# Kernel optimization log

Measured on AMD Instinct MI355X. Metric: run time of the kernel, lower is better.

Reference implementation:

```python
import jax, jax.numpy as jnp
import numpy as np

B, I, H, AH, AI = 4096, 1024, 1024, 128, 16
EPS = 1e-5  # nn.LayerNorm default


def _ln(x, w, b):
    mu = jnp.mean(x, -1, keepdims=True)
    var = jnp.mean((x - mu) ** 2, -1, keepdims=True)
    return (x - mu) * jax.lax.rsqrt(var + EPS) * w + b


def setup_inputs() -> dict:
    key = jax.random.key(0)
    ks = jax.random.split(key, 12)
    d = {}
    d['x'] = jax.random.normal(ks[0], (B, I), jnp.float32)
    d['total_h'] = jax.random.normal(ks[1], (B, H + AH), jnp.float32)
    d['total_c'] = jax.random.normal(ks[2], (B, H + AH), jnp.float32)
    # main cell params
    d['w_ih'] = jax.random.normal(ks[3], (4 * H, I), jnp.float32) * 0.02
    d['w_hh'] = jax.random.normal(ks[4], (4 * H, H), jnp.float32) * 0.02
    d['b_ih'] = jnp.zeros((4 * H,), jnp.float32)
    d['b_hh'] = jnp.zeros((4 * H,), jnp.float32)
    d['ln_i_w'] = jnp.ones((4 * H,), jnp.float32); d['ln_i_b'] = jnp.zeros((4 * H,), jnp.float32)
    d['ln_h_w'] = jnp.ones((4 * H,), jnp.float32); d['ln_h_b'] = jnp.zeros((4 * H,), jnp.float32)
    d['ln_c_w'] = jnp.ones((H,), jnp.float32); d['ln_c_b'] = jnp.zeros((H,), jnp.float32)
    # 8 AdaptiveNorm modules, stacked on leading axis (order ix,jx,fx,ox,ih,jh,fh,oh)
    d['norm_zw_w'] = jax.random.normal(ks[5], (8, AI, AH), jnp.float32) * 0.05
    d['norm_zw_b'] = jnp.ones((8, AI), jnp.float32)
    d['norm_alpha_w'] = jax.random.normal(ks[6], (8, H, AI), jnp.float32) * (0.1 / AI)
    # 8 AdaptiveBias modules, stacked (order ixb,jxb,fxb,oxb,ihb,jhb,fhb,ohb)
    d['bias_zb_w'] = jax.random.normal(ks[7], (8, AI, AH), jnp.float32) * 0.01
    d['bias_beta_w'] = jax.random.normal(ks[8], (8, H, AI), jnp.float32) * 0.01
    # adaptive LayerNormLSTMCell (input = I+H, hidden = AH)
    d['a_w_ih'] = jax.random.normal(ks[9], (4 * AH, I + H), jnp.float32) * 0.02
    d['a_w_hh'] = jax.random.normal(ks[10], (4 * AH, AH), jnp.float32) * 0.02
    d['a_ln_i_w'] = jnp.ones((4 * AH,), jnp.float32); d['a_ln_i_b'] = jnp.zeros((4 * AH,), jnp.float32)
    d['a_ln_h_w'] = jnp.ones((4 * AH,), jnp.float32); d['a_ln_h_b'] = jnp.zeros((4 * AH,), jnp.float32)
    d['a_ln_c_w'] = jnp.ones((AH,), jnp.float32); d['a_ln_c_b'] = jnp.zeros((AH,), jnp.float32)
    return d


def _forward(x, total_h, total_c, w_ih, w_hh, b_ih, b_hh, ln_i_w, ln_i_b,
             ln_h_w, ln_h_b, ln_c_w, ln_c_b, norm_zw_w, norm_zw_b,
             norm_alpha_w, bias_zb_w, bias_beta_w, a_w_ih, a_w_hh,
             a_ln_i_w, a_ln_i_b, a_ln_h_w, a_ln_h_b, a_ln_c_w, a_ln_c_b):
    hx, ah = total_h[:, :H], total_h[:, H:]
    cx, ac = total_c[:, :H], total_c[:, H:]
    # ---- adaptive LayerNormLSTMCell (hypernetwork) ----
    ai = jnp.concatenate([x, hx], axis=1)                     # [B, I+H]
    ig = _ln(ai @ a_w_ih.T, a_ln_i_w, a_ln_i_b)               # [B, 4*AH]
    hg = _ln(ah @ a_w_hh.T, a_ln_h_w, a_ln_h_b)
    g = ig + hg
    gi, gf, gj, go = jnp.split(g, 4, axis=1)                  # ingate, forget, cell, out
    acy = _ln(jax.nn.sigmoid(gf) * ac + jax.nn.sigmoid(gi) * jnp.tanh(gj), a_ln_c_w, a_ln_c_b)
    ada = jax.nn.sigmoid(go) * jnp.tanh(acy)                  # adaptive_output [B, AH]
    # ---- 8 AdaptiveNorm scales + 8 AdaptiveBias offsets, batched ----
    zw = jnp.einsum('ba,sia->bsi', ada, norm_zw_w) + norm_zw_b  # [B,8,AI]
    alpha = jnp.einsum('bsi,shi->bsh', zw, norm_alpha_w)        # [B,8,H]
    zb = jnp.einsum('ba,sia->bsi', ada, bias_zb_w)              # [B,8,AI]
    beta = jnp.einsum('bsi,shi->bsh', zb, bias_beta_w)          # [B,8,H]
    xh = (x @ w_ih.T).reshape(-1, 4, H)                         # chunks ix,jx,fx,ox
    hh = (hx @ w_hh.T).reshape(-1, 4, H)                        # chunks ih,jh,fh,oh
    in_g = (xh * alpha[:, :4] + b_ih.reshape(4, H) + beta[:, :4]).reshape(-1, 4 * H)
    hid_g = (hh * alpha[:, 4:] + b_hh.reshape(4, H) + beta[:, 4:]).reshape(-1, 4 * H)
    # ---- cell_operate ----
    gates = _ln(in_g, ln_i_w, ln_i_b) + _ln(hid_g, ln_h_w, ln_h_b)
    i, j, f, o = jnp.split(gates, 4, axis=1)                  # in, cell, forget, out
    cy = _ln(jax.nn.sigmoid(f) * cx + jax.nn.sigmoid(i) * jnp.tanh(j), ln_c_w, ln_c_b)
    hy = jax.nn.sigmoid(o) * jnp.tanh(cy)
    new_total_h = jnp.concatenate([hy, ada], axis=1)
    new_total_c = jnp.concatenate([cy, acy], axis=1)
    return hy, new_total_h, new_total_c


def reference(x, total_h, total_c, w_ih, w_hh, b_ih, b_hh, ln_i_w, ln_i_b,
              ln_h_w, ln_h_b, ln_c_w, ln_c_b, norm_zw_w, norm_zw_b,
              norm_alpha_w, bias_zb_w, bias_beta_w, a_w_ih, a_w_hh,
              a_ln_i_w, a_ln_i_b, a_ln_h_w, a_ln_h_b, a_ln_c_w, a_ln_c_b):
    return _forward(x, total_h, total_c, w_ih, w_hh, b_ih, b_hh, ln_i_w, ln_i_b,
                    ln_h_w, ln_h_b, ln_c_w, ln_c_b, norm_zw_w, norm_zw_b,
                    norm_alpha_w, bias_zb_w, bias_beta_w, a_w_ih, a_w_hh,
                    a_ln_i_w, a_ln_i_b, a_ln_h_w, a_ln_h_b, a_ln_c_w, a_ln_c_b)
```

## Files before the change

### kernel.cpp

```cpp
#include <hip/hip_runtime.h>
#include <cstdint>
#include <cstddef>


#define B_   4096
#define I_   1024
#define H_   1024
#define AH_  128
#define G4_  4096
#define EPS_ 1e-5f

#define OUT_TH ((size_t)B_ * H_)
#define OUT_TC (OUT_TH + (size_t)B_ * (H_ + AH_))

typedef short s16x8 __attribute__((ext_vector_type(8)));
typedef float f32x4 __attribute__((ext_vector_type(4)));

__device__ __forceinline__ unsigned short f2bf_rn(float f) {
    unsigned int u = __builtin_bit_cast(unsigned int, f);
    unsigned int r = u + 0x7FFFu + ((u >> 16) & 1u);
    return (unsigned short)(r >> 16);
}
__device__ __forceinline__ float bf2f(unsigned short h) {
    unsigned int u = ((unsigned int)h) << 16;
    return __builtin_bit_cast(float, u);
}
__device__ __forceinline__ float sigf(float x) { return 1.0f / (1.0f + expf(-x)); }

__device__ __forceinline__ void gld16(const void* g, void* l) {
    __builtin_amdgcn_global_load_lds(
        (const __attribute__((address_space(1))) unsigned int*)g,
        (__attribute__((address_space(3))) unsigned int*)l,
        16, 0, 0);
}

__global__ void split8_kernel(const float* __restrict__ src, int srcStride, int srcOff,
                              long nThreads, int kshift,
                              unsigned short* __restrict__ dst, int dstStride,
                              int offHi, int offLo) {
    long t = (long)blockIdx.x * blockDim.x + threadIdx.x;
    if (t >= nThreads) return;
    int r  = (int)(t >> kshift);
    int kk = ((int)t & ((1 << kshift) - 1)) * 8;
    const float* sp = src + (size_t)r * srcStride + srcOff + kk;
    f32x4 v0 = *(const f32x4*)sp;
    f32x4 v1 = *(const f32x4*)(sp + 4);
    float v[8] = {v0[0], v0[1], v0[2], v0[3], v1[0], v1[1], v1[2], v1[3]};
    s16x8 hi, lo;
#pragma unroll
    for (int j = 0; j < 8; ++j) {
        unsigned short hu = f2bf_rn(v[j]);
        unsigned short lu = f2bf_rn(v[j] - bf2f(hu));
        hi[j] = (short)hu; lo[j] = (short)lu;
    }
    size_t base = (size_t)r * dstStride + kk;
    *(s16x8*)(dst + base + offHi) = hi;
    *(s16x8*)(dst + base + offLo) = lo;
}

__global__ void transpose128_kernel(const float* __restrict__ zw_w, const float* __restrict__ zb_w,
                                    float* __restrict__ ZWT, float* __restrict__ ZBT) {
    int t = blockIdx.x * 256 + threadIdx.x;
    int idx = t >> 7, a = t & 127;
    ZWT[a * 128 + idx] = zw_w[idx * 128 + a];
    ZBT[a * 128 + idx] = zb_w[idx * 128 + a];
}

__launch_bounds__(256, 2)
__global__ void gemm_bt_bf16(const unsigned short* __restrict__ A0,
                             const unsigned short* __restrict__ A1,
                             int lda,
                             const unsigned short* __restrict__ W, int ldw, int wzOff,
                             float* __restrict__ C, int ldc, long czOff,
                             int K, int kA1, int kW1) {
    __shared__ __align__(16) unsigned short As[128 * 32];
    __shared__ __align__(16) unsigned short Bs[128 * 32];
    const unsigned short* A  = blockIdx.z ? A1 : A0;
    const unsigned short* Wp = W + (size_t)blockIdx.z * wzOff;
    float* Cp = C + (size_t)blockIdx.z * czOff;

    const int gx = gridDim.x;
    int lin = blockIdx.y * gx + blockIdx.x;
    const int cpx = (gx * gridDim.y) >> 3;
    lin = (lin & 7) * cpx + (lin >> 3);
    const int bx = lin % gx, by = lin / gx;

    const int tid  = threadIdx.x;
    const int lane = tid & 63;
    const int w    = tid >> 6;
    const int wr   = w >> 1, wc = w & 1;
    const int l15  = lane & 15;
    const int lk   = (lane >> 4) * 8;

    f32x4 acc[4][4] = {};

    for (int kt = 0; kt < K; kt += 32) {
        const unsigned short* Ab = A  + (kt < kA1 ? kt : kt - kA1);
        const unsigned short* Wb = Wp + (kt < kW1 ? kt : kt - kW1);
#pragma unroll
        for (int it = 0; it < 2; ++it) {
            int q = it * 256 + tid;
            int row = q >> 2, c8 = (q & 3) * 8;
            gld16(Ab + (size_t)(by * 128 + row) * lda + c8,
                  (char*)As + (size_t)(it * 256 + w * 64) * 16);
        }
#pragma unroll
        for (int it = 0; it < 2; ++it) {
            int q = it * 256 + tid;
            int row = q >> 2, c8 = (q & 3) * 8;
            gld16(Wb + (size_t)(bx * 128 + row) * ldw + c8,
                  (char*)Bs + (size_t)(it * 256 + w * 64) * 16);
        }
        __syncthreads();

        s16x8 afr[4], bfr[4];
#pragma unroll
        for (int m = 0; m < 4; ++m)
            afr[m] = *(const s16x8*)&As[(wr * 64 + m * 16 + l15) * 32 + lk];
#pragma unroll
        for (int n = 0; n < 4; ++n)
            bfr[n] = *(const s16x8*)&Bs[(wc * 64 + n * 16 + l15) * 32 + lk];
#pragma unroll
        for (int m = 0; m < 4; ++m)
#pragma unroll
            for (int n = 0; n < 4; ++n)
                acc[m][n] = __builtin_amdgcn_mfma_f32_16x16x32_bf16(
                    afr[m], bfr[n], acc[m][n], 0, 0, 0);
        __syncthreads();
    }

    const int r0 = by * 128 + wr * 64;
    const int c0 = bx * 128 + wc * 64;
    const int rl = (lane >> 4) * 4;
#pragma unroll
    for (int m = 0; m < 4; ++m)
#pragma unroll
        for (int n = 0; n < 4; ++n)
#pragma unroll
            for (int j = 0; j < 4; ++j)
                Cp[(size_t)(r0 + m * 16 + rl + j) * ldc + c0 + n * 16 + l15] = acc[m][n][j];
}

__launch_bounds__(64)
__global__ void adaptive_gates_kernel(const float* __restrict__ IGa, const float* __restrict__ IGb,
                                      const float* __restrict__ HG,
                                      const float* __restrict__ total_c,
                                      const float* __restrict__ alniw, const float* __restrict__ alnib,
                                      const float* __restrict__ alnhw, const float* __restrict__ alnhb,
                                      const float* __restrict__ alncw, const float* __restrict__ alncb,
                                      const float* __restrict__ ZWT, const float* __restrict__ zw_b,
                                      const float* __restrict__ ZBT,
                                      float* __restrict__ ZW, float* __restrict__ ZB,
                                      float* __restrict__ out) {
    const int b    = blockIdx.x;
    const int lane = threadIdx.x;
    __shared__ float ada_lds[AH_];

    float ig[8], hg[8];
    const float* ipa = IGa + (size_t)b * 512 + lane * 8;
    const float* ipb = IGb + (size_t)b * 512 + lane * 8;
    const float* hgp = HG  + (size_t)b * 512 + lane * 8;
    float sI = 0, qI = 0, sH = 0, qH = 0;
#pragma unroll
    for (int j = 0; j < 8; ++j) {
        ig[j] = ipa[j] + ipb[j]; sI += ig[j]; qI += ig[j] * ig[j];
        hg[j] = hgp[j];          sH += hg[j]; qH += hg[j] * hg[j];
    }
#pragma unroll
    for (int m = 1; m < 64; m <<= 1) {
        sI += __shfl_xor(sI, m); qI += __shfl_xor(qI, m);
        sH += __shfl_xor(sH, m); qH += __shfl_xor(qH, m);
    }
    const float muI = sI * (1.0f / 512.0f);
    const float rI  = rsqrtf(qI * (1.0f / 512.0f) - muI * muI + EPS_);
    const float muH = sH * (1.0f / 512.0f);
    const float rH  = rsqrtf(qH * (1.0f / 512.0f) - muH * muH + EPS_);

    float g[8];
#pragma unroll
    for (int j = 0; j < 8; ++j) {
        int c = lane * 8 + j;
        g[j] = (ig[j] - muI) * rI * alniw[c] + alnib[c]
             + (hg[j] - muH) * rH * alnhw[c] + alnhb[c];
    }

    const int l15 = lane & 15;
    float cp[8], gov[8];
    float s = 0, q = 0;
#pragma unroll
    for (int j = 0; j < 8; ++j) {
        float giv = __shfl(g[j], l15);
        float gfv = __shfl(g[j], 16 + l15);
        float gjv = __shfl(g[j], 32 + l15);
        gov[j]    = __shfl(g[j], 48 + l15);
        int a = l15 * 8 + j;
        float ac = total_c[(size_t)b * (H_ + AH_) + H_ + a];
        cp[j] = sigf(gfv) * ac + sigf(giv) * tanhf(gjv);
        s += cp[j]; q += cp[j] * cp[j];
    }
#pragma unroll
    for (int m = 1; m < 16; m <<= 1) { s += __shfl_xor(s, m); q += __shfl_xor(q, m); }
    const float mu = s * (1.0f / 128.0f);
    const float rs = rsqrtf(q * (1.0f / 128.0f) - mu * mu + EPS_);

    float adav[8], acyv[8];
#pragma unroll
    for (int j = 0; j < 8; ++j) {
        int a = l15 * 8 + j;
        acyv[j] = (cp[j] - mu) * rs * alncw[a] + alncb[a];
        adav[j] = sigf(gov[j]) * tanhf(acyv[j]);
    }
    if (lane < 16) {
#pragma unroll
        for (int j = 0; j < 8; ++j) {
            int a = lane * 8 + j;
            ada_lds[a] = adav[j];
            out[OUT_TH + (size_t)b * (H_ + AH_) + H_ + a] = adav[j];
            out[OUT_TC + (size_t)b * (H_ + AH_) + H_ + a] = acyv[j];
        }
    }
    __syncthreads();

    float az0 = 0, az1 = 0, ab0 = 0, ab1 = 0;
#pragma unroll 4
    for (int a = 0; a < 128; ++a) {
        float ad = ada_lds[a];
        float2 wz = *(const float2*)&ZWT[a * 128 + lane * 2];
        float2 wb = *(const float2*)&ZBT[a * 128 + lane * 2];
        az0 += ad * wz.x; az1 += ad * wz.y;
        ab0 += ad * wb.x; ab1 += ad * wb.y;
    }
    const int i0 = lane * 2, i1 = lane * 2 + 1;
    ZW[(size_t)b * 128 + i0] = az0 + zw_b[i0];
    ZW[(size_t)b * 128 + i1] = az1 + zw_b[i1];
    ZB[(size_t)b * 128 + i0] = ab0;
    ZB[(size_t)b * 128 + i1] = ab1;
}

__launch_bounds__(512)
__global__ void scale_stats_kernel(float* __restrict__ XH, float* __restrict__ HH,
                                   const float* __restrict__ ZW, const float* __restrict__ ZB,
                                   const float* __restrict__ aw, const float* __restrict__ bw,
                                   const float* __restrict__ b_ih, const float* __restrict__ b_hh,
                                   float* __restrict__ STATS) {
    const int tid  = threadIdx.x;
    const int lane = tid & 63;
    const int w    = tid >> 6;
    const int b0   = blockIdx.x * 8;

    __shared__ __align__(16) float zwl[8 * 128], zbl[8 * 128];
    __shared__ float part[8][8][4];
    __shared__ float tot[8][4];

    for (int t = tid; t < 1024; t += 512) {
        int r = t >> 7, si = t & 127;
        zwl[t] = ZW[(size_t)(b0 + r) * 128 + si];
        zbl[t] = ZB[(size_t)(b0 + r) * 128 + si];
    }
    __syncthreads();

    float sI[8] = {}, qI[8] = {}, sH[8] = {}, qH[8] = {};

    for (int strip = w; strip < 128; strip += 8) {
        const bool isIn = strip < 64;
        const int  c    = (isIn ? strip : strip - 64) * 64 + lane;
        const int  se   = (c >> 10) + (isIn ? 0 : 4);
        float*       X    = isIn ? XH : HH;
        const float* bias = isIn ? b_ih : b_hh;
        const int    h    = c & 1023;

        const f32x4* awp = (const f32x4*)(aw + ((size_t)se * 1024 + h) * 16);
        const f32x4* bwp = (const f32x4*)(bw + ((size_t)se * 1024 + h) * 16);
        f32x4 a0 = awp[0], a1 = awp[1], a2 = awp[2], a3 = awp[3];
        f32x4 w0 = bwp[0], w1 = bwp[1], w2 = bwp[2], w3 = bwp[3];
        const float bc = bias[c];

#pragma unroll
        for (int r = 0; r < 8; ++r) {
            const f32x4* zp = (const f32x4*)&zwl[r * 128 + se * 16];
            const f32x4* yp = (const f32x4*)&zbl[r * 128 + se * 16];
            f32x4 z0 = zp[0], z1 = zp[1], z2 = zp[2], z3 = zp[3];
            f32x4 y0 = yp[0], y1 = yp[1], y2 = yp[2], y3 = yp[3];
            float alpha = a0[0]*z0[0] + a0[1]*z0[1] + a0[2]*z0[2] + a0[3]*z0[3]
                        + a1[0]*z1[0] + a1[1]*z1[1] + a1[2]*z1[2] + a1[3]*z1[3]
                        + a2[0]*z2[0] + a2[1]*z2[1] + a2[2]*z2[2] + a2[3]*z2[3]
                        + a3[0]*z3[0] + a3[1]*z3[1] + a3[2]*z3[2] + a3[3]*z3[3];
            float beta  = w0[0]*y0[0] + w0[1]*y0[1] + w0[2]*y0[2] + w0[3]*y0[3]
                        + w1[0]*y1[0] + w1[1]*y1[1] + w1[2]*y1[2] + w1[3]*y1[3]
                        + w2[0]*y2[0] + w2[1]*y2[1] + w2[2]*y2[2] + w2[3]*y2[3]
                        + w3[0]*y3[0] + w3[1]*y3[1] + w3[2]*y3[2] + w3[3]*y3[3];
            size_t off = (size_t)(b0 + r) * G4_ + c;
            float v = X[off] * alpha + bc + beta;
            X[off] = v;
            if (isIn) { sI[r] += v; qI[r] += v * v; }
            else      { sH[r] += v; qH[r] += v * v; }
        }
    }

#pragma unroll
    for (int r = 0; r < 8; ++r) {
#pragma unroll
        for (int m = 1; m < 64; m <<= 1) {
            sI[r] += __shfl_xor(sI[r], m); qI[r] += __shfl_xor(qI[r], m);
            sH[r] += __shfl_xor(sH[r], m); qH[r] += __shfl_xor(qH[r], m);
        }
        if (lane == 0) {
            part[w][r][0] = sI[r]; part[w][r][1] = qI[r];
            part[w][r][2] = sH[r]; part[w][r][3] = qH[r];
        }
    }
    __syncthreads();
    if (tid < 32) {
        int r = tid >> 2, cmp = tid & 3;
        float t = 0;
        for (int ww = 0; ww < 8; ++ww) t += part[ww][r][cmp];
        tot[r][cmp] = t;
    }
    __syncthreads();
    if (tid < 8) {
        int r = tid;
        float muI = tot[r][0] * (1.0f / 4096.0f);
        float vI  = tot[r][1] * (1.0f / 4096.0f) - muI * muI;
        float muH = tot[r][2] * (1.0f / 4096.0f);
        float vH  = tot[r][3] * (1.0f / 4096.0f) - muH * muH;
        f32x4 st = { muI, rsqrtf(vI + EPS_), muH, rsqrtf(vH + EPS_) };
        *(f32x4*)(STATS + (size_t)(b0 + r) * 4) = st;
    }
}

__launch_bounds__(256)
__global__ void final_gates_kernel(const float* __restrict__ XH, const float* __restrict__ HH,
                                   const float* __restrict__ STATS,
                                   const float* __restrict__ lniw, const float* __restrict__ lnib,
                                   const float* __restrict__ lnhw, const float* __restrict__ lnhb,
                                   const float* __restrict__ lncw, const float* __restrict__ lncb,
                                   const float* __restrict__ total_c,
                                   float* __restrict__ out) {
    const int b = blockIdx.x, tid = threadIdx.x;
    const int lane = tid & 63, w = tid >> 6;
    __shared__ float red[4][2];

    const f32x4 st = *(const f32x4*)(STATS + (size_t)b * 4);
    const int h0 = tid * 4;

    float gg[4][4];
#pragma unroll
    for (int s = 0; s < 4; ++s) {
        int c = s * 1024 + h0;
        f32x4 xi = *(const f32x4*)(XH + (size_t)b * G4_ + c);
        f32x4 hi = *(const f32x4*)(HH + (size_t)b * G4_ + c);
        f32x4 wi = *(const f32x4*)(lniw + c);
        f32x4 bi = *(const f32x4*)(lnib + c);
        f32x4 wh = *(const f32x4*)(lnhw + c);
        f32x4 bh = *(const f32x4*)(lnhb + c);
#pragma unroll
        for (int e = 0; e < 4; ++e)
            gg[s][e] = (xi[e] - st[0]) * st[1] * wi[e] + bi[e]
                     + (hi[e] - st[2]) * st[3] * wh[e] + bh[e];
    }

    float cp[4], ov[4];
    float s_ = 0, q_ = 0;
#pragma unroll
    for (int e = 0; e < 4; ++e) {
        float iv = gg[0][e], jv = gg[1][e], fv = gg[2][e];
        ov[e] = gg[3][e];
        float cx = total_c[(size_t)b * (H_ + AH_) + h0 + e];
        cp[e] = sigf(fv) * cx + sigf(iv) * tanhf(jv);
        s_ += cp[e]; q_ += cp[e] * cp[e];
    }
#pragma unroll
    for (int m = 1; m < 64; m <<= 1) { s_ += __shfl_xor(s_, m); q_ += __shfl_xor(q_, m); }
    if (lane == 0) { red[w][0] = s_; red[w][1] = q_; }
    __syncthreads();
    float S = red[0][0] + red[1][0] + red[2][0] + red[3][0];
    float Q = red[0][1] + red[1][1] + red[2][1] + red[3][1];
    float mu = S * (1.0f / 1024.0f);
    float rs = rsqrtf(Q * (1.0f / 1024.0f) - mu * mu + EPS_);

    f32x4 hyv, cyv;
#pragma unroll
    for (int e = 0; e < 4; ++e) {
        int h = h0 + e;
        float cy = (cp[e] - mu) * rs * lncw[h] + lncb[h];
        float hy = sigf(ov[e]) * tanhf(cy);
        cyv[e] = cy; hyv[e] = hy;
    }
    *(f32x4*)(out + (size_t)b * H_ + h0)                  = hyv;
    *(f32x4*)(out + OUT_TH + (size_t)b * (H_ + AH_) + h0) = hyv;
    *(f32x4*)(out + OUT_TC + (size_t)b * (H_ + AH_) + h0) = cyv;
}

extern "C" void kernel_launch(void* const* d_in, const int* in_sizes, int n_in,
                              void* d_out, int out_size, void* d_ws, size_t ws_size,
                              hipStream_t stream) {
    const float* x          = (const float*)d_in[0];
    const float* total_h    = (const float*)d_in[1];
    const float* total_c    = (const float*)d_in[2];
    const float* w_ih       = (const float*)d_in[3];
    const float* w_hh       = (const float*)d_in[4];
    const float* b_ih       = (const float*)d_in[5];
    const float* b_hh       = (const float*)d_in[6];
    const float* ln_i_w     = (const float*)d_in[7];
    const float* ln_i_b     = (const float*)d_in[8];
    const float* ln_h_w     = (const float*)d_in[9];
    const float* ln_h_b     = (const float*)d_in[10];
    const float* ln_c_w     = (const float*)d_in[11];
    const float* ln_c_b     = (const float*)d_in[12];
    const float* norm_zw_w  = (const float*)d_in[13];
    const float* norm_zw_b  = (const float*)d_in[14];
    const float* norm_alpha_w = (const float*)d_in[15];
    const float* bias_zb_w  = (const float*)d_in[16];
    const float* bias_beta_w = (const float*)d_in[17];
    const float* a_w_ih     = (const float*)d_in[18];
    const float* a_w_hh     = (const float*)d_in[19];
    const float* a_ln_i_w   = (const float*)d_in[20];
    const float* a_ln_i_b   = (const float*)d_in[21];
    const float* a_ln_h_w   = (const float*)d_in[22];
    const float* a_ln_h_b   = (const float*)d_in[23];
    const float* a_ln_c_w   = (const float*)d_in[24];
    const float* a_ln_c_b   = (const float*)d_in[25];
    float* out = (float*)d_out;

    char* ws = (char*)d_ws;
    unsigned short* XA  = (unsigned short*)(ws + 0);
    unsigned short* HXA = (unsigned short*)(ws + 16777216);
    unsigned short* WIH = (unsigned short*)(ws + 33554432);
    unsigned short* WHH = (unsigned short*)(ws + 50331648);
    unsigned short* WAI = (unsigned short*)(ws + 67108864);
    unsigned short* AHS = (unsigned short*)(ws + 71303168);
    unsigned short* WAH = (unsigned short*)(ws + 73400320);
    float* IG    = (float*)(ws + 73662464);
    float* HG    = (float*)(ws + 90439680);
    float* XHp   = (float*)(ws + 98828288);
    float* HHp   = (float*)(ws + 165937152);
    float* ZW    = (float*)(ws + 233046016);
    float* ZB    = (float*)(ws + 235143168);
    float* STATS = (float*)(ws + 237240320);
    float* ZWT   = (float*)(ws + 237305856);
    float* ZBT   = (float*)(ws + 237371392);

    auto grid8 = [](long n) { return dim3((unsigned)((n / 8 + 255) / 256)); };

    split8_kernel<<<grid8(4096L*1024), 256, 0, stream>>>(x,       1024, 0,    4096L*128, 7, XA,  2048, 0, 1024);
    split8_kernel<<<grid8(4096L*1024), 256, 0, stream>>>(total_h, 1152, 0,    4096L*128, 7, HXA, 2048, 0, 1024);
    split8_kernel<<<grid8(4096L*128),  256, 0, stream>>>(total_h, 1152, 1024, 4096L*16,  4, AHS, 256,  0, 128);
    split8_kernel<<<grid8(4096L*1024), 256, 0, stream>>>(w_ih,    1024, 0,    4096L*128, 7, WIH, 2048, 0, 1024);
    split8_kernel<<<grid8(4096L*1024), 256, 0, stream>>>(w_hh,    1024, 0,    4096L*128, 7, WHH, 2048, 0, 1024);
    split8_kernel<<<grid8(512L*1024),  256, 0, stream>>>(a_w_ih,  2048, 0,    512L*128,  7, WAI, 4096, 0,    1024);
    split8_kernel<<<grid8(512L*1024),  256, 0, stream>>>(a_w_ih,  2048, 1024, 512L*128,  7, WAI, 4096, 2048, 3072);
    split8_kernel<<<grid8(512L*128),   256, 0, stream>>>(a_w_hh,  128,  0,    512L*16,   4, WAH, 256,  0, 128);
    transpose128_kernel<<<64, 256, 0, stream>>>(norm_zw_w, bias_zb_w, ZWT, ZBT);

    gemm_bt_bf16<<<dim3(4, 32, 2), 256, 0, stream>>>(XA, HXA, 2048, WAI, 4096, 2048, IG, 512, 4096L*512, 3072, 1024, 2048);
    gemm_bt_bf16<<<dim3(4, 32, 1), 256, 0, stream>>>(AHS, AHS, 256, WAH, 256, 0, HG, 512, 0, 384, 128, 256);
    gemm_bt_bf16<<<dim3(32, 32, 1), 256, 0, stream>>>(XA,  XA,  2048, WIH, 2048, 0, XHp, 4096, 0, 3072, 1024, 2048);
    gemm_bt_bf16<<<dim3(32, 32, 1), 256, 0, stream>>>(HXA, HXA, 2048, WHH, 2048, 0, HHp, 4096, 0, 3072, 1024, 2048);

    adaptive_gates_kernel<<<4096, 64, 0, stream>>>(IG, IG + 4096L*512, HG, total_c,
        a_ln_i_w, a_ln_i_b, a_ln_h_w, a_ln_h_b, a_ln_c_w, a_ln_c_b,
        ZWT, norm_zw_b, ZBT, ZW, ZB, out);

    scale_stats_kernel<<<512, 512, 0, stream>>>(XHp, HHp, ZW, ZB,
        norm_alpha_w, bias_beta_w, b_ih, b_hh, STATS);

    final_gates_kernel<<<4096, 256, 0, stream>>>(XHp, HHp, STATS,
        ln_i_w, ln_i_b, ln_h_w, ln_h_b, ln_c_w, ln_c_b, total_c, out);
}
```

Measured before the change: 668.6 us.

## Fuse adaptive scale/bias and LayerNorm partial stats into main GEMM epilogue

The scale_stats kernel is removed. Its per-column alpha/beta scaling, bias add and row sum/sumsq partials move into the epilogue of the two large GEMMs, which are now merged into one z=2 launch that runs after the adaptive gates kernel. This saves a full read-modify-write pass over the two 64MB gate buffers and one launch. The final kernel reduces 128 partial pairs per row to get mean and rstd. The cost is a heavier epilogue with extra global loads of alpha/beta weights, and the big GEMMs can no longer overlap with the adaptive path.

```diff
diff --git a/kernel.cpp b/kernel.cpp
--- a/kernel.cpp
+++ b/kernel.cpp
@@ -26,6 +26,9 @@
     return __builtin_bit_cast(float, u);
 }
 __device__ __forceinline__ float sigf(float x) { return 1.0f / (1.0f + expf(-x)); }
+__device__ __forceinline__ float dot4(f32x4 a, f32x4 b) {
+    return a[0]*b[0] + a[1]*b[1] + a[2]*b[2] + a[3]*b[3];
+}
 
 __device__ __forceinline__ void gld16(const void* g, void* l) {
     __builtin_amdgcn_global_load_lds(
@@ -72,12 +75,17 @@
                              int lda,
                              const unsigned short* __restrict__ W, int ldw, int wzOff,
                              float* __restrict__ C, int ldc, long czOff,
-                             int K, int kA1, int kW1) {
+                             int K, int kA1, int kW1,
+                             const float* __restrict__ ZW, const float* __restrict__ ZB,
+                             const float* __restrict__ aw, const float* __restrict__ bw,
+                             const float* __restrict__ biasX, const float* __restrict__ biasH,
+                             float* __restrict__ PART) {
     __shared__ __align__(16) unsigned short As[128 * 32];
     __shared__ __align__(16) unsigned short Bs[128 * 32];
-    const unsigned short* A  = blockIdx.z ? A1 : A0;
-    const unsigned short* Wp = W + (size_t)blockIdx.z * wzOff;
-    float* Cp = C + (size_t)blockIdx.z * czOff;
+    const int z = blockIdx.z;
+    const unsigned short* A  = z ? A1 : A0;
+    const unsigned short* Wp = W + (size_t)z * wzOff;
+    float* Cp = C + (size_t)z * czOff;
 
     const int gx = gridDim.x;
     int lin = blockIdx.y * gx + blockIdx.x;
@@ -91,6 +99,7 @@
     const int wr   = w >> 1, wc = w & 1;
     const int l15  = lane & 15;
     const int lk   = (lane >> 4) * 8;
+    const int rl   = (lane >> 4) * 4;
 
     f32x4 acc[4][4] = {};
 
@@ -129,16 +138,83 @@
         __syncthreads();
     }
 
-    const int r0 = by * 128 + wr * 64;
-    const int c0 = bx * 128 + wc * 64;
-    const int rl = (lane >> 4) * 4;
-#pragma unroll
-    for (int m = 0; m < 4; ++m)
-#pragma unroll
-        for (int n = 0; n < 4; ++n)
-#pragma unroll
-            for (int j = 0; j < 4; ++j)
-                Cp[(size_t)(r0 + m * 16 + rl + j) * ldc + c0 + n * 16 + l15] = acc[m][n][j];
+    if (PART == nullptr) {
+        const int r0 = by * 128 + wr * 64;
+        const int c0 = bx * 128 + wc * 64;
+#pragma unroll
+        for (int m = 0; m < 4; ++m)
+#pragma unroll
+            for (int n = 0; n < 4; ++n)
+#pragma unroll
+                for (int j = 0; j < 4; ++j)
+                    Cp[(size_t)(r0 + m * 16 + rl + j) * ldc + c0 + n * 16 + l15] = acc[m][n][j];
+        return;
+    }
+
+    const int se = (z ? 4 : 0) + (bx >> 3);
+    float* zwl = (float*)As;
+    float* zbl = (float*)Bs;
+    {
+        int rr = tid >> 1, ii = (tid & 1) * 8;
+        const float* zp = ZW + (size_t)(by * 128 + rr) * 128 + se * 16 + ii;
+        const float* yp = ZB + (size_t)(by * 128 + rr) * 128 + se * 16 + ii;
+        f32x4 za = *(const f32x4*)zp, zc = *(const f32x4*)(zp + 4);
+        f32x4 ya = *(const f32x4*)yp, yc = *(const f32x4*)(yp + 4);
+        *(f32x4*)&zwl[rr * 16 + ii]     = za;
+        *(f32x4*)&zwl[rr * 16 + ii + 4] = zc;
+        *(f32x4*)&zbl[rr * 16 + ii]     = ya;
+        *(f32x4*)&zbl[rr * 16 + ii + 4] = yc;
+    }
+    __syncthreads();
+
+    const float* bias = z ? biasH : biasX;
+#pragma unroll
+    for (int half = 0; half < 2; ++half) {
+        f32x4 awv[2][4], bwv[2][4];
+        float bcv[2];
+        int   ccol[2];
+#pragma unroll
+        for (int t = 0; t < 2; ++t) {
+            int cc = bx * 128 + wc * 64 + (half * 2 + t) * 16 + l15;
+            ccol[t] = cc;
+            int h = cc & 1023;
+            const f32x4* ap = (const f32x4*)(aw + ((size_t)se * 1024 + h) * 16);
+            const f32x4* bp = (const f32x4*)(bw + ((size_t)se * 1024 + h) * 16);
+            awv[t][0] = ap[0]; awv[t][1] = ap[1]; awv[t][2] = ap[2]; awv[t][3] = ap[3];
+            bwv[t][0] = bp[0]; bwv[t][1] = bp[1]; bwv[t][2] = bp[2]; bwv[t][3] = bp[3];
+            bcv[t] = bias[cc];
+        }
+#pragma unroll
+        for (int m = 0; m < 4; ++m)
+#pragma unroll
+        for (int j = 0; j < 4; ++j) {
+            const int rloc = wr * 64 + m * 16 + rl + j;
+            const f32x4* zp = (const f32x4*)&zwl[rloc * 16];
+            const f32x4* yp = (const f32x4*)&zbl[rloc * 16];
+            f32x4 z0 = zp[0], z1 = zp[1], z2 = zp[2], z3 = zp[3];
+            f32x4 y0 = yp[0], y1 = yp[1], y2 = yp[2], y3 = yp[3];
+            float s = 0, q = 0;
+#pragma unroll
+            for (int t = 0; t < 2; ++t) {
+                float alpha = dot4(z0, awv[t][0]) + dot4(z1, awv[t][1])
+                            + dot4(z2, awv[t][2]) + dot4(z3, awv[t][3]);
+                float beta  = dot4(y0, bwv[t][0]) + dot4(y1, bwv[t][1])
+                            + dot4(y2, bwv[t][2]) + dot4(y3, bwv[t][3]);
+                float v = acc[m][half * 2 + t][j] * alpha + bcv[t] + beta;
+                Cp[(size_t)(by * 128 + rloc) * ldc + ccol[t]] = v;
+                s += v; q += v * v;
+            }
+#pragma unroll
+            for (int msk = 1; msk < 16; msk <<= 1) {
+                s += __shfl_xor(s, msk); q += __shfl_xor(q, msk);
+            }
+            if (l15 == 0) {
+                int cb = bx * 4 + wc * 2 + half;
+                float2 pr = { s, q };
+                *(float2*)&PART[(((size_t)z * 4096 + by * 128 + rloc) * 128 + cb) * 2] = pr;
+            }
+        }
+    }
 }
 
 __launch_bounds__(64)
@@ -237,100 +313,9 @@
     ZB[(size_t)b * 128 + i1] = ab1;
 }
 
-__launch_bounds__(512)
-__global__ void scale_stats_kernel(float* __restrict__ XH, float* __restrict__ HH,
-                                   const float* __restrict__ ZW, const float* __restrict__ ZB,
-                                   const float* __restrict__ aw, const float* __restrict__ bw,
-                                   const float* __restrict__ b_ih, const float* __restrict__ b_hh,
-                                   float* __restrict__ STATS) {
-    const int tid  = threadIdx.x;
-    const int lane = tid & 63;
-    const int w    = tid >> 6;
-    const int b0   = blockIdx.x * 8;
-
-    __shared__ __align__(16) float zwl[8 * 128], zbl[8 * 128];
-    __shared__ float part[8][8][4];
-    __shared__ float tot[8][4];
-
-    for (int t = tid; t < 1024; t += 512) {
-        int r = t >> 7, si = t & 127;
-        zwl[t] = ZW[(size_t)(b0 + r) * 128 + si];
-        zbl[t] = ZB[(size_t)(b0 + r) * 128 + si];
-    }
-    __syncthreads();
-
-    float sI[8] = {}, qI[8] = {}, sH[8] = {}, qH[8] = {};
-
-    for (int strip = w; strip < 128; strip += 8) {
-        const bool isIn = strip < 64;
-        const int  c    = (isIn ? strip : strip - 64) * 64 + lane;
-        const int  se   = (c >> 10) + (isIn ? 0 : 4);
-        float*       X    = isIn ? XH : HH;
-        const float* bias = isIn ? b_ih : b_hh;
-        const int    h    = c & 1023;
-
-        const f32x4* awp = (const f32x4*)(aw + ((size_t)se * 1024 + h) * 16);
-        const f32x4* bwp = (const f32x4*)(bw + ((size_t)se * 1024 + h) * 16);
-        f32x4 a0 = awp[0], a1 = awp[1], a2 = awp[2], a3 = awp[3];
-        f32x4 w0 = bwp[0], w1 = bwp[1], w2 = bwp[2], w3 = bwp[3];
-        const float bc = bias[c];
-
-#pragma unroll
-        for (int r = 0; r < 8; ++r) {
-            const f32x4* zp = (const f32x4*)&zwl[r * 128 + se * 16];
-            const f32x4* yp = (const f32x4*)&zbl[r * 128 + se * 16];
-            f32x4 z0 = zp[0], z1 = zp[1], z2 = zp[2], z3 = zp[3];
-            f32x4 y0 = yp[0], y1 = yp[1], y2 = yp[2], y3 = yp[3];
-            float alpha = a0[0]*z0[0] + a0[1]*z0[1] + a0[2]*z0[2] + a0[3]*z0[3]
-                        + a1[0]*z1[0] + a1[1]*z1[1] + a1[2]*z1[2] + a1[3]*z1[3]
-                        + a2[0]*z2[0] + a2[1]*z2[1] + a2[2]*z2[2] + a2[3]*z2[3]
-                        + a3[0]*z3[0] + a3[1]*z3[1] + a3[2]*z3[2] + a3[3]*z3[3];
-            float beta  = w0[0]*y0[0] + w0[1]*y0[1] + w0[2]*y0[2] + w0[3]*y0[3]
-                        + w1[0]*y1[0] + w1[1]*y1[1] + w1[2]*y1[2] + w1[3]*y1[3]
-                        + w2[0]*y2[0] + w2[1]*y2[1] + w2[2]*y2[2] + w2[3]*y2[3]
-                        + w3[0]*y3[0] + w3[1]*y3[1] + w3[2]*y3[2] + w3[3]*y3[3];
-            size_t off = (size_t)(b0 + r) * G4_ + c;
-            float v = X[off] * alpha + bc + beta;
-            X[off] = v;
-            if (isIn) { sI[r] += v; qI[r] += v * v; }
-            else      { sH[r] += v; qH[r] += v * v; }
-        }
-    }
-
-#pragma unroll
-    for (int r = 0; r < 8; ++r) {
-#pragma unroll
-        for (int m = 1; m < 64; m <<= 1) {
-            sI[r] += __shfl_xor(sI[r], m); qI[r] += __shfl_xor(qI[r], m);
-            sH[r] += __shfl_xor(sH[r], m); qH[r] += __shfl_xor(qH[r], m);
-        }
-        if (lane == 0) {
-            part[w][r][0] = sI[r]; part[w][r][1] = qI[r];
-            part[w][r][2] = sH[r]; part[w][r][3] = qH[r];
-        }
-    }
-    __syncthreads();
-    if (tid < 32) {
-        int r = tid >> 2, cmp = tid & 3;
-        float t = 0;
-        for (int ww = 0; ww < 8; ++ww) t += part[ww][r][cmp];
-        tot[r][cmp] = t;
-    }
-    __syncthreads();
-    if (tid < 8) {
-        int r = tid;
-        float muI = tot[r][0] * (1.0f / 4096.0f);
-        float vI  = tot[r][1] * (1.0f / 4096.0f) - muI * muI;
-        float muH = tot[r][2] * (1.0f / 4096.0f);
-        float vH  = tot[r][3] * (1.0f / 4096.0f) - muH * muH;
-        f32x4 st = { muI, rsqrtf(vI + EPS_), muH, rsqrtf(vH + EPS_) };
-        *(f32x4*)(STATS + (size_t)(b0 + r) * 4) = st;
-    }
-}
-
 __launch_bounds__(256)
 __global__ void final_gates_kernel(const float* __restrict__ XH, const float* __restrict__ HH,
-                                   const float* __restrict__ STATS,
+                                   const float* __restrict__ PART,
                                    const float* __restrict__ lniw, const float* __restrict__ lnib,
                                    const float* __restrict__ lnhw, const float* __restrict__ lnhb,
                                    const float* __restrict__ lncw, const float* __restrict__ lncb,
@@ -339,10 +324,23 @@
     const int b = blockIdx.x, tid = threadIdx.x;
     const int lane = tid & 63, w = tid >> 6;
     __shared__ float red[4][2];
-
-    const f32x4 st = *(const f32x4*)(STATS + (size_t)b * 4);
+    __shared__ float red2[2][2];
+
+    if (w < 2) {
+        const float* pz = PART + ((size_t)w * 4096 + b) * 256;
+        f32x4 v = *(const f32x4*)(pz + lane * 4);
+        float s = v[0] + v[2], q = v[1] + v[3];
+#pragma unroll
+        for (int m = 1; m < 64; m <<= 1) { s += __shfl_xor(s, m); q += __shfl_xor(q, m); }
+        if (lane == 0) { red2[w][0] = s; red2[w][1] = q; }
+    }
+    __syncthreads();
+    const float muI = red2[0][0] * (1.0f / 4096.0f);
+    const float rI  = rsqrtf(red2[0][1] * (1.0f / 4096.0f) - muI * muI + EPS_);
+    const float muH = red2[1][0] * (1.0f / 4096.0f);
+    const float rH  = rsqrtf(red2[1][1] * (1.0f / 4096.0f) - muH * muH + EPS_);
+
     const int h0 = tid * 4;
-
     float gg[4][4];
 #pragma unroll
     for (int s = 0; s < 4; ++s) {
@@ -355,8 +353,8 @@
         f32x4 bh = *(const f32x4*)(lnhb + c);
 #pragma unroll
         for (int e = 0; e < 4; ++e)
-            gg[s][e] = (xi[e] - st[0]) * st[1] * wi[e] + bi[e]
-                     + (hi[e] - st[2]) * st[3] * wh[e] + bh[e];
+            gg[s][e] = (xi[e] - muI) * rI * wi[e] + bi[e]
+                     + (hi[e] - muH) * rH * wh[e] + bh[e];
     }
 
     float cp[4], ov[4];
@@ -436,9 +434,9 @@
     float* HHp   = (float*)(ws + 165937152);
     float* ZW    = (float*)(ws + 233046016);
     float* ZB    = (float*)(ws + 235143168);
-    float* STATS = (float*)(ws + 237240320);
-    float* ZWT   = (float*)(ws + 237305856);
-    float* ZBT   = (float*)(ws + 237371392);
+    float* ZWT   = (float*)(ws + 237240320);
+    float* ZBT   = (float*)(ws + 237305856);
+    float* PART  = (float*)(ws + 237371392);
 
     auto grid8 = [](long n) { return dim3((unsigned)((n / 8 + 255) / 256)); };
 
@@ -452,18 +450,21 @@
     split8_kernel<<<grid8(512L*128),   256, 0, stream>>>(a_w_hh,  128,  0,    512L*16,   4, WAH, 256,  0, 128);
     transpose128_kernel<<<64, 256, 0, stream>>>(norm_zw_w, bias_zb_w, ZWT, ZBT);
 
-    gemm_bt_bf16<<<dim3(4, 32, 2), 256, 0, stream>>>(XA, HXA, 2048, WAI, 4096, 2048, IG, 512, 4096L*512, 3072, 1024, 2048);
-    gemm_bt_bf16<<<dim3(4, 32, 1), 256, 0, stream>>>(AHS, AHS, 256, WAH, 256, 0, HG, 512, 0, 384, 128, 256);
-    gemm_bt_bf16<<<dim3(32, 32, 1), 256, 0, stream>>>(XA,  XA,  2048, WIH, 2048, 0, XHp, 4096, 0, 3072, 1024, 2048);
-    gemm_bt_bf16<<<dim3(32, 32, 1), 256, 0, stream>>>(HXA, HXA, 2048, WHH, 2048, 0, HHp, 4096, 0, 3072, 1024, 2048);
+    gemm_bt_bf16<<<dim3(4, 32, 2), 256, 0, stream>>>(XA, HXA, 2048, WAI, 4096, 2048,
+        IG, 512, 4096L*512, 3072, 1024, 2048,
+        nullptr, nullptr, nullptr, nullptr, nullptr, nullptr, nullptr);
+    gemm_bt_bf16<<<dim3(4, 32, 1), 256, 0, stream>>>(AHS, AHS, 256, WAH, 256, 0,
+        HG, 512, 0, 384, 128, 256,
+        nullptr, nullptr, nullptr, nullptr, nullptr, nullptr, nullptr);
 
     adaptive_gates_kernel<<<4096, 64, 0, stream>>>(IG, IG + 4096L*512, HG, total_c,
         a_ln_i_w, a_ln_i_b, a_ln_h_w, a_ln_h_b, a_ln_c_w, a_ln_c_b,
         ZWT, norm_zw_b, ZBT, ZW, ZB, out);
 
-    scale_stats_kernel<<<512, 512, 0, stream>>>(XHp, HHp, ZW, ZB,
-        norm_alpha_w, bias_beta_w, b_ih, b_hh, STATS);
-
-    final_gates_kernel<<<4096, 256, 0, stream>>>(XHp, HHp, STATS,
+    gemm_bt_bf16<<<dim3(32, 32, 2), 256, 0, stream>>>(XA, HXA, 2048, WIH, 2048, 8388608,
+        XHp, 4096, 16777216, 3072, 1024, 2048,
+        ZW, ZB, norm_alpha_w, bias_beta_w, b_ih, b_hh, PART);
+
+    final_gates_kernel<<<4096, 256, 0, stream>>>(XHp, HHp, PART,
         ln_i_w, ln_i_b, ln_h_w, ln_h_b, ln_c_w, ln_c_b, total_c, out);
 }
```

Measured after the change: 723.1 us. +8.1%, slower.

## Fuse split/transpose prep into one kernel and widen scale_stats to two columns per lane

Applied to the files above, without the earlier changes.

Merges the eight bf16 hi/lo split launches and the transpose launch into a single prep kernel that dispatches on block index, removing per-launch overhead and tail gaps. The scale_stats kernel now has each lane handle two adjacent columns with float2 loads and stores, reusing the shared-memory z vectors across both columns and halving the strip loop count. The big GEMMs are also reordered to run after the adaptive-gates kernel. The costs are more registers per thread in scale_stats and a larger branchy prep grid.

```diff
diff --git a/kernel.cpp b/kernel.cpp
--- a/kernel.cpp
+++ b/kernel.cpp
@@ -26,6 +26,9 @@
     return __builtin_bit_cast(float, u);
 }
 __device__ __forceinline__ float sigf(float x) { return 1.0f / (1.0f + expf(-x)); }
+__device__ __forceinline__ float dot4(f32x4 a, f32x4 b) {
+    return a[0]*b[0] + a[1]*b[1] + a[2]*b[2] + a[3]*b[3];
+}
 
 __device__ __forceinline__ void gld16(const void* g, void* l) {
     __builtin_amdgcn_global_load_lds(
@@ -34,14 +37,12 @@
         16, 0, 0);
 }
 
-__global__ void split8_kernel(const float* __restrict__ src, int srcStride, int srcOff,
-                              long nThreads, int kshift,
-                              unsigned short* __restrict__ dst, int dstStride,
-                              int offHi, int offLo) {
-    long t = (long)blockIdx.x * blockDim.x + threadIdx.x;
-    if (t >= nThreads) return;
-    int r  = (int)(t >> kshift);
-    int kk = ((int)t & ((1 << kshift) - 1)) * 8;
+__device__ __forceinline__ void split_body(const float* __restrict__ src, int srcStride,
+                                           int srcOff, int kshift,
+                                           unsigned short* __restrict__ dst, int dstStride,
+                                           int offHi, int offLo, int t) {
+    int r  = t >> kshift;
+    int kk = (t & ((1 << kshift) - 1)) * 8;
     const float* sp = src + (size_t)r * srcStride + srcOff + kk;
     f32x4 v0 = *(const f32x4*)sp;
     f32x4 v1 = *(const f32x4*)(sp + 4);
@@ -58,12 +59,38 @@
     *(s16x8*)(dst + base + offLo) = lo;
 }
 
-__global__ void transpose128_kernel(const float* __restrict__ zw_w, const float* __restrict__ zb_w,
-                                    float* __restrict__ ZWT, float* __restrict__ ZBT) {
-    int t = blockIdx.x * 256 + threadIdx.x;
-    int idx = t >> 7, a = t & 127;
-    ZWT[a * 128 + idx] = zw_w[idx * 128 + a];
-    ZBT[a * 128 + idx] = zb_w[idx * 128 + a];
+__global__ void prep_kernel(const float* __restrict__ x, const float* __restrict__ total_h,
+                            const float* __restrict__ w_ih, const float* __restrict__ w_hh,
+                            const float* __restrict__ a_w_ih, const float* __restrict__ a_w_hh,
+                            const float* __restrict__ zw_w, const float* __restrict__ zb_w,
+                            unsigned short* __restrict__ XA, unsigned short* __restrict__ HXA,
+                            unsigned short* __restrict__ WIH, unsigned short* __restrict__ WHH,
+                            unsigned short* __restrict__ WAI, unsigned short* __restrict__ AHS,
+                            unsigned short* __restrict__ WAH,
+                            float* __restrict__ ZWT, float* __restrict__ ZBT) {
+    const int bid = blockIdx.x, tid = threadIdx.x;
+    if (bid < 2048) {
+        split_body(x, 1024, 0, 7, XA, 2048, 0, 1024, bid * 256 + tid);
+    } else if (bid < 4096) {
+        split_body(total_h, 1152, 0, 7, HXA, 2048, 0, 1024, (bid - 2048) * 256 + tid);
+    } else if (bid < 6144) {
+        split_body(w_ih, 1024, 0, 7, WIH, 2048, 0, 1024, (bid - 4096) * 256 + tid);
+    } else if (bid < 8192) {
+        split_body(w_hh, 1024, 0, 7, WHH, 2048, 0, 1024, (bid - 6144) * 256 + tid);
+    } else if (bid < 8448) {
+        split_body(total_h, 1152, 1024, 4, AHS, 256, 0, 128, (bid - 8192) * 256 + tid);
+    } else if (bid < 8704) {
+        split_body(a_w_ih, 2048, 0, 7, WAI, 4096, 0, 1024, (bid - 8448) * 256 + tid);
+    } else if (bid < 8960) {
+        split_body(a_w_ih, 2048, 1024, 7, WAI, 4096, 2048, 3072, (bid - 8704) * 256 + tid);
+    } else if (bid < 8992) {
+        split_body(a_w_hh, 128, 0, 4, WAH, 256, 0, 128, (bid - 8960) * 256 + tid);
+    } else {
+        int t = (bid - 8992) * 256 + tid;
+        int idx = t >> 7, a = t & 127;
+        ZWT[a * 128 + idx] = zw_w[idx * 128 + a];
+        ZBT[a * 128 + idx] = zb_w[idx * 128 + a];
+    }
 }
 
 __launch_bounds__(256, 2)
@@ -237,7 +264,7 @@
     ZB[(size_t)b * 128 + i1] = ab1;
 }
 
-__launch_bounds__(512)
+__launch_bounds__(512, 1)
 __global__ void scale_stats_kernel(float* __restrict__ XH, float* __restrict__ HH,
                                    const float* __restrict__ ZW, const float* __restrict__ ZB,
                                    const float* __restrict__ aw, const float* __restrict__ bw,
@@ -261,19 +288,21 @@
 
     float sI[8] = {}, qI[8] = {}, sH[8] = {}, qH[8] = {};
 
-    for (int strip = w; strip < 128; strip += 8) {
-        const bool isIn = strip < 64;
-        const int  c    = (isIn ? strip : strip - 64) * 64 + lane;
+    for (int strip = w; strip < 64; strip += 8) {
+        const bool isIn = strip < 32;
+        const int  c    = (isIn ? strip : strip - 32) * 128 + lane * 2;
         const int  se   = (c >> 10) + (isIn ? 0 : 4);
         float*       X    = isIn ? XH : HH;
         const float* bias = isIn ? b_ih : b_hh;
         const int    h    = c & 1023;
 
-        const f32x4* awp = (const f32x4*)(aw + ((size_t)se * 1024 + h) * 16);
-        const f32x4* bwp = (const f32x4*)(bw + ((size_t)se * 1024 + h) * 16);
-        f32x4 a0 = awp[0], a1 = awp[1], a2 = awp[2], a3 = awp[3];
-        f32x4 w0 = bwp[0], w1 = bwp[1], w2 = bwp[2], w3 = bwp[3];
-        const float bc = bias[c];
+        const f32x4* ap = (const f32x4*)(aw + ((size_t)se * 1024 + h) * 16);
+        const f32x4* bp = (const f32x4*)(bw + ((size_t)se * 1024 + h) * 16);
+        f32x4 A0 = ap[0], A1 = ap[1], A2 = ap[2], A3 = ap[3];
+        f32x4 A4 = ap[4], A5 = ap[5], A6 = ap[6], A7 = ap[7];
+        f32x4 B0 = bp[0], B1 = bp[1], B2 = bp[2], B3 = bp[3];
+        f32x4 B4 = bp[4], B5 = bp[5], B6 = bp[6], B7 = bp[7];
+        const float2 bc = *(const float2*)&bias[c];
 
 #pragma unroll
         for (int r = 0; r < 8; ++r) {
@@ -281,19 +310,19 @@
             const f32x4* yp = (const f32x4*)&zbl[r * 128 + se * 16];
             f32x4 z0 = zp[0], z1 = zp[1], z2 = zp[2], z3 = zp[3];
             f32x4 y0 = yp[0], y1 = yp[1], y2 = yp[2], y3 = yp[3];
-            float alpha = a0[0]*z0[0] + a0[1]*z0[1] + a0[2]*z0[2] + a0[3]*z0[3]
-                        + a1[0]*z1[0] + a1[1]*z1[1] + a1[2]*z1[2] + a1[3]*z1[3]
-                        + a2[0]*z2[0] + a2[1]*z2[1] + a2[2]*z2[2] + a2[3]*z2[3]
-                        + a3[0]*z3[0] + a3[1]*z3[1] + a3[2]*z3[2] + a3[3]*z3[3];
-            float beta  = w0[0]*y0[0] + w0[1]*y0[1] + w0[2]*y0[2] + w0[3]*y0[3]
-                        + w1[0]*y1[0] + w1[1]*y1[1] + w1[2]*y1[2] + w1[3]*y1[3]
-                        + w2[0]*y2[0] + w2[1]*y2[1] + w2[2]*y2[2] + w2[3]*y2[3]
-                        + w3[0]*y3[0] + w3[1]*y3[1] + w3[2]*y3[2] + w3[3]*y3[3];
+            float alpha0 = dot4(z0, A0) + dot4(z1, A1) + dot4(z2, A2) + dot4(z3, A3);
+            float alpha1 = dot4(z0, A4) + dot4(z1, A5) + dot4(z2, A6) + dot4(z3, A7);
+            float beta0  = dot4(y0, B0) + dot4(y1, B1) + dot4(y2, B2) + dot4(y3, B3);
+            float beta1  = dot4(y0, B4) + dot4(y1, B5) + dot4(y2, B6) + dot4(y3, B7);
             size_t off = (size_t)(b0 + r) * G4_ + c;
-            float v = X[off] * alpha + bc + beta;
-            X[off] = v;
-            if (isIn) { sI[r] += v; qI[r] += v * v; }
-            else      { sH[r] += v; qH[r] += v * v; }
+            float2 xv = *(const float2*)&X[off];
+            float v0 = xv.x * alpha0 + bc.x + beta0;
+            float v1 = xv.y * alpha1 + bc.y + beta1;
+            float2 vv = { v0, v1 };
+            *(float2*)&X[off] = vv;
+            float sv = v0 + v1, qv = v0 * v0 + v1 * v1;
+            if (isIn) { sI[r] += sv; qI[r] += qv; }
+            else      { sH[r] += sv; qH[r] += qv; }
         }
     }
 
@@ -440,27 +469,23 @@
     float* ZWT   = (float*)(ws + 237305856);
     float* ZBT   = (float*)(ws + 237371392);
 
-    auto grid8 = [](long n) { return dim3((unsigned)((n / 8 + 255) / 256)); };
-
-    split8_kernel<<<grid8(4096L*1024), 256, 0, stream>>>(x,       1024, 0,    4096L*128, 7, XA,  2048, 0, 1024);
-    split8_kernel<<<grid8(4096L*1024), 256, 0, stream>>>(total_h, 1152, 0,    4096L*128, 7, HXA, 2048, 0, 1024);
-    split8_kernel<<<grid8(4096L*128),  256, 0, stream>>>(total_h, 1152, 1024, 4096L*16,  4, AHS, 256,  0, 128);
-    split8_kernel<<<grid8(4096L*1024), 256, 0, stream>>>(w_ih,    1024, 0,    4096L*128, 7, WIH, 2048, 0, 1024);
-    split8_kernel<<<grid8(4096L*1024), 256, 0, stream>>>(w_hh,    1024, 0,    4096L*128, 7, WHH, 2048, 0, 1024);
-    split8_kernel<<<grid8(512L*1024),  256, 0, stream>>>(a_w_ih,  2048, 0,    512L*128,  7, WAI, 4096, 0,    1024);
-    split8_kernel<<<grid8(512L*1024),  256, 0, stream>>>(a_w_ih,  2048, 1024, 512L*128,  7, WAI, 4096, 2048, 3072);
-    split8_kernel<<<grid8(512L*128),   256, 0, stream>>>(a_w_hh,  128,  0,    512L*16,   4, WAH, 256,  0, 128);
-    transpose128_kernel<<<64, 256, 0, stream>>>(norm_zw_w, bias_zb_w, ZWT, ZBT);
-
-    gemm_bt_bf16<<<dim3(4, 32, 2), 256, 0, stream>>>(XA, HXA, 2048, WAI, 4096, 2048, IG, 512, 4096L*512, 3072, 1024, 2048);
-    gemm_bt_bf16<<<dim3(4, 32, 1), 256, 0, stream>>>(AHS, AHS, 256, WAH, 256, 0, HG, 512, 0, 384, 128, 256);
-    gemm_bt_bf16<<<dim3(32, 32, 1), 256, 0, stream>>>(XA,  XA,  2048, WIH, 2048, 0, XHp, 4096, 0, 3072, 1024, 2048);
-    gemm_bt_bf16<<<dim3(32, 32, 1), 256, 0, stream>>>(HXA, HXA, 2048, WHH, 2048, 0, HHp, 4096, 0, 3072, 1024, 2048);
+    prep_kernel<<<9056, 256, 0, stream>>>(x, total_h, w_ih, w_hh, a_w_ih, a_w_hh,
+        norm_zw_w, bias_zb_w, XA, HXA, WIH, WHH, WAI, AHS, WAH, ZWT, ZBT);
+
+    gemm_bt_bf16<<<dim3(4, 32, 2), 256, 0, stream>>>(XA, HXA, 2048, WAI, 4096, 2048,
+        IG, 512, 4096L*512, 3072, 1024, 2048);
+    gemm_bt_bf16<<<dim3(4, 32, 1), 256, 0, stream>>>(AHS, AHS, 256, WAH, 256, 0,
+        HG, 512, 0, 384, 128, 256);
 
     adaptive_gates_kernel<<<4096, 64, 0, stream>>>(IG, IG + 4096L*512, HG, total_c,
         a_ln_i_w, a_ln_i_b, a_ln_h_w, a_ln_h_b, a_ln_c_w, a_ln_c_b,
         ZWT, norm_zw_b, ZBT, ZW, ZB, out);
 
+    gemm_bt_bf16<<<dim3(32, 32, 1), 256, 0, stream>>>(XA,  XA,  2048, WIH, 2048, 0,
+        XHp, 4096, 0, 3072, 1024, 2048);
+    gemm_bt_bf16<<<dim3(32, 32, 1), 256, 0, stream>>>(HXA, HXA, 2048, WHH, 2048, 0,
+        HHp, 4096, 0, 3072, 1024, 2048);
+
     scale_stats_kernel<<<512, 512, 0, stream>>>(XHp, HHp, ZW, ZB,
         norm_alpha_w, bias_beta_w, b_ih, b_hh, STATS);
 
```

Measured after the change: 687.8 us. +2.9%, slower.
